# Kernel optimization log

Hardware: AMD Instinct MI355X
Metric: run time of the kernel (lower is better)

## Reference

```python
import jax, jax.numpy as jnp
import numpy as np

B, S, H, F, E, K = 4, 2048, 1024, 3584, 8, 2
CAP_FACTOR = 1.25


def setup_inputs() -> dict:
    key = jax.random.key(0)
    k1, k2, k3, k4, k5 = jax.random.split(key, 5)
    s_h = 1.0 / np.sqrt(H)
    s_f = 1.0 / np.sqrt(F)
    return {
        "hidden_states": jax.random.normal(k1, (B, S, H), dtype=jnp.float32),
        "gate_w": jax.random.normal(k2, (E, H), dtype=jnp.float32) * s_h,
        "w1": jax.random.normal(k3, (E, H, F), dtype=jnp.float32) * s_h,
        "w2": jax.random.normal(k4, (E, F, H), dtype=jnp.float32) * s_f,
        "w3": jax.random.normal(k5, (E, H, F), dtype=jnp.float32) * s_h,
    }


def _moe_forward(hidden_states, gate_w, w1, w2, w3):
    b, s, h = hidden_states.shape
    dtype = hidden_states.dtype
    x = hidden_states.reshape(-1, h)  # [B*S, H]
    router_logits = x @ gate_w.T  # [B*S, E]
    expert_weights = jax.nn.softmax(router_logits.astype(jnp.float32), axis=1)
    _, selected_experts = jax.lax.top_k(expert_weights, K)  # [B*S, K]

    top_k_idx = selected_experts.reshape(b, s, K)
    probs = expert_weights.reshape(b, s, E)

    capacity = int(s * K / E * CAP_FACTOR)  # expert capacity per batch

    # dispatch/combine masks (Mixtral 'dropping' implementation)
    expert_mask = jax.nn.one_hot(top_k_idx, E, dtype=jnp.int32)  # [b,s,K,E]
    mask_fused = expert_mask.reshape(b, s * K, E)
    count_fused = jnp.cumsum(mask_fused, axis=1)  # running count per expert
    count = count_fused.reshape(b, s, K, E)
    trunc_mask = expert_mask * (count <= capacity).astype(jnp.int32)
    combined_mask = trunc_mask.sum(axis=2)  # [b,s,E]
    masked_probs = probs * combined_mask  # drop over-capacity tokens

    pos_fused = mask_fused * count_fused
    pos = pos_fused.reshape(b, s, K, E)
    combined_pos = pos.sum(axis=2) * combined_mask  # [b,s,E], 1-based slot
    pos_in_cap = jax.nn.one_hot(combined_pos, capacity + 1, dtype=jnp.int32)
    combine_mask = masked_probs[..., None] * pos_in_cap  # [b,s,E,cap+1]
    combine_mask = combine_mask[..., 1:].astype(dtype)  # drop slot 0 (dropped tokens)
    dispatch_mask = (combine_mask != 0).astype(dtype)  # [b,s,E,cap]

    # dispatch tokens into per-expert capacity buffers
    dispatch = jnp.einsum('bsm,bsec->ebcm', hidden_states, dispatch_mask)
    # expert FFN (SwiGLU)
    h1 = jnp.einsum('ebcm,emh->ebch', dispatch, w1)
    h3 = jnp.einsum('ebcm,emh->ebch', dispatch, w3)
    expert_out = jnp.einsum('ebch,ehm->ebcm', jax.nn.silu(h1) * h3, w2)
    # combine back to token order with routing probabilities
    final = jnp.einsum('ebcm,bsec->bsm', expert_out, combine_mask)
    return final


def reference(hidden_states, gate_w, w1, w2, w3):
    return _moe_forward(hidden_states, gate_w, w1, w2, w3)
```

## Files before the change

### kernel.cpp

```cpp
#include <hip/hip_runtime.h>
#include <hip/hip_bf16.h>
#include <math.h>

#define B_   4
#define S_   2048
#define H_   1024
#define F_   3584
#define E_   8
#define TOPK 2
#define CAP  640
#define M_   (B_*CAP)
#define NTOK (B_*S_)

typedef __attribute__((ext_vector_type(8))) short short8;
typedef __attribute__((ext_vector_type(4))) float f32x4;
typedef __attribute__((ext_vector_type(4))) unsigned short us4;

static __device__ __forceinline__ unsigned short f2bf(float f) {
  __hip_bfloat16 h = __float2bfloat16(f);
  return *reinterpret_cast<unsigned short*>(&h);
}
static __device__ __forceinline__ float bf2f(unsigned short u) {
  unsigned int x = ((unsigned int)u) << 16;
  float f;
  __builtin_memcpy(&f, &x, 4);
  return f;
}

static __device__ __forceinline__ void gload16(const void* g, void* l) {
  __builtin_amdgcn_global_load_lds((const __attribute__((address_space(1))) void*)g,
                                   (__attribute__((address_space(3))) void*)l, 16, 0, 0);
}

#define BAR() __builtin_amdgcn_s_barrier()
#define WLG() asm volatile("s_waitcnt lgkmcnt(0)" ::: "memory")

__global__ __launch_bounds__(64) void k_router(const float* __restrict__ hs,
                                               const float* __restrict__ gw,
                                               int* __restrict__ e01,
                                               float* __restrict__ p01) {
  int t = blockIdx.x;
  int lane = threadIdx.x;
  const float4* xv = (const float4*)(hs + (size_t)t * H_);
  float4 xr[4];
#pragma unroll
  for (int i = 0; i < 4; ++i) xr[i] = xv[lane + i * 64];
  float logit[E_];
#pragma unroll
  for (int e = 0; e < E_; ++e) {
    const float4* gv = (const float4*)(gw + (size_t)e * H_);
    float acc = 0.f;
#pragma unroll
    for (int i = 0; i < 4; ++i) {
      float4 g = gv[lane + i * 64];
      acc += xr[i].x * g.x + xr[i].y * g.y + xr[i].z * g.z + xr[i].w * g.w;
    }
#pragma unroll
    for (int off = 32; off > 0; off >>= 1) acc += __shfl_xor(acc, off);
    logit[e] = acc;
  }
  float mx = logit[0];
#pragma unroll
  for (int e = 1; e < E_; ++e) mx = fmaxf(mx, logit[e]);
  float p[E_], s = 0.f;
#pragma unroll
  for (int e = 0; e < E_; ++e) { p[e] = expf(logit[e] - mx); s += p[e]; }
  float inv = 1.f / s;
  int e0 = 0;
#pragma unroll
  for (int e = 1; e < E_; ++e) if (p[e] > p[e0]) e0 = e;
  int e1 = (e0 == 0) ? 1 : 0;
#pragma unroll
  for (int e = 0; e < E_; ++e) if (e != e0 && p[e] > p[e1]) e1 = e;
  if (lane == 0) {
    e01[t * 2 + 0] = e0;
    e01[t * 2 + 1] = e1;
    p01[t * 2 + 0] = p[e0] * inv;
    p01[t * 2 + 1] = p[e1] * inv;
  }
}

__global__ __launch_bounds__(256) void k_positions(const int* __restrict__ e01,
                                                   int* __restrict__ pos,
                                                   int* __restrict__ disp) {
  int b = blockIdx.x, tid = threadIdx.x;
  __shared__ unsigned char eid[S_ * TOPK];
  __shared__ int part[256];
  for (int i = tid; i < E_ * CAP; i += 256)
    disp[((size_t)(i / CAP) * B_ + b) * CAP + (i % CAP)] = -1;
  for (int i = tid; i < S_ * TOPK; i += 256)
    eid[i] = (unsigned char)e01[b * S_ * TOPK + i];
  __syncthreads();
  const int per = (S_ * TOPK) / 256;
  int base = tid * per;
  for (int e = 0; e < E_; ++e) {
    int cnt = 0;
    for (int j = 0; j < per; ++j) cnt += (eid[base + j] == e) ? 1 : 0;
    part[tid] = cnt;
    __syncthreads();
    for (int off = 1; off < 256; off <<= 1) {
      int v = part[tid];
      int add = (tid >= off) ? part[tid - off] : 0;
      __syncthreads();
      part[tid] = v + add;
      __syncthreads();
    }
    int run = part[tid] - cnt;
    for (int j = 0; j < per; ++j) {
      int sl = base + j;
      if (eid[sl] == e) {
        ++run;
        int p = (run <= CAP) ? (run - 1) : -1;
        pos[b * S_ * TOPK + sl] = p;
        if (p >= 0) disp[((size_t)e * B_ + b) * CAP + p] = sl >> 1;
      }
    }
    __syncthreads();
  }
}

__global__ __launch_bounds__(256) void k_transpose(const float* __restrict__ in,
                                                   unsigned short* __restrict__ outp,
                                                   int R, int C, int ileave, int half,
                                                   size_t ostride_e) {
  __shared__ unsigned short ls[64][72];
  int e = blockIdx.z, tc = blockIdx.x, tr = blockIdx.y, tid = threadIdx.x;
  const float* src = in + (size_t)e * R * C + (size_t)tr * 64 * C + (size_t)tc * 64;
#pragma unroll
  for (int i = 0; i < 16; ++i) {
    int row = i * 4 + (tid >> 6), col = tid & 63;
    ls[row][col] = f2bf(src[(size_t)row * C + col]);
  }
  __syncthreads();
  unsigned short* dbase = outp + (size_t)e * ostride_e;
#pragma unroll
  for (int i = 0; i < 4; ++i) {
    int orow = i * 16 + (tid >> 4), oc = (tid & 15) * 4;
    int gr = tc * 64 + orow;
    int ri = ileave ? ((gr & ~15) * 2 + (gr & 15) + half * 16) : gr;
    us4 v = {ls[oc + 0][orow], ls[oc + 1][orow], ls[oc + 2][orow], ls[oc + 3][orow]};
    *(us4*)&dbase[(size_t)ri * R + tr * 64 + oc] = v;
  }
}

__global__ __launch_bounds__(256) void k_dispatch(const float* __restrict__ hs,
                                                  const int* __restrict__ disp,
                                                  unsigned short* __restrict__ xd) {
  int slot = blockIdx.x;
  int tid = threadIdx.x;
  int tok = disp[slot];
  int b = (slot / CAP) % B_;
  us4 v;
  if (tok >= 0) {
    const float4* src = (const float4*)(hs + ((size_t)b * S_ + tok) * H_);
    float4 f = src[tid];
    v = {f2bf(f.x), f2bf(f.y), f2bf(f.z), f2bf(f.w)};
  } else {
    v = {0, 0, 0, 0};
  }
  *(us4*)&xd[(size_t)slot * H_ + tid * 4] = v;
}

#define STAGE_A(d, h, t) {                                                    \
    int _ro = ((d) * 2 + (h)) * 8192 + tid * 8;                               \
    const unsigned short* _p = srcA + (size_t)(t) * 64 + (h) * 32;            \
    gload16(_p, &lds[_ro]);                                                   \
    gload16(_p + (size_t)128 * KTOT, &lds[_ro + 4096]);                       \
  }
#define STAGE_B(d, h, t) {                                                    \
    int _ro = 32768 + ((d) * 2 + (h)) * BREG + tid * 8;                       \
    const unsigned short* _p = srcB + (size_t)(t) * 64 + (h) * 32;            \
    gload16(_p, &lds[_ro]);                                                   \
    if (NREG == 4) gload16(_p + (size_t)128 * KTOT, &lds[_ro + 4096]);        \
  }
#define RD_A(d, h) {                                                          \
    const unsigned short* _pa = &lds[((d) * 2 + (h)) * 8192 + aoff];          \
    _Pragma("unroll") for (int m = 0; m < 8; ++m)                             \
      a[m] = *(const short8*)&_pa[m * 512];                                   \
  }
#define RD_B(d, h) {                                                          \
    const unsigned short* _pb = &lds[32768 + ((d) * 2 + (h)) * BREG + boff];  \
    _Pragma("unroll") for (int n = 0; n < NREG; ++n)                          \
      bfr[n] = *(const short8*)&_pb[n * 512];                                 \
  }
#define MFMA_ALL() {                                                          \
    __builtin_amdgcn_s_setprio(1);                                            \
    _Pragma("unroll") for (int m = 0; m < 8; ++m)                             \
      _Pragma("unroll") for (int n = 0; n < NREG; ++n)                        \
        acc[m][n] = __builtin_amdgcn_mfma_f32_16x16x32_bf16(a[m], bfr[n], acc[m][n], 0, 0, 0); \
    __builtin_amdgcn_s_setprio(0);                                            \
  }
#define WVM() {                                                               \
    if (NREG == 4) asm volatile("s_waitcnt vmcnt(8)" ::: "memory");           \
    else           asm volatile("s_waitcnt vmcnt(6)" ::: "memory");           \
  }
#define PHASE(pd, ph, sd, sh, st) {                                           \
    RD_A(pd, ph); RD_B(pd, ph);                                               \
    STAGE_A(sd, sh, st); STAGE_B(sd, sh, st);                                 \
    asm volatile("s_waitcnt lgkmcnt(8)" ::: "memory");                        \
    BAR(); WLG();                                                             \
    MFMA_ALL();                                                               \
    WVM(); BAR();                                                             \
  }

template <int KTOT, bool SWIGLU, int NREG, int MT, int NTN, int NTOTB>
__global__ __launch_bounds__(512, 2) void k_gemm256(const unsigned short* __restrict__ Aall,
                                                    const unsigned short* __restrict__ Ball,
                                                    unsigned short* __restrict__ Cout) {
  constexpr int NT = KTOT / 64;
  constexpr int NI = NT / 2;
  constexpr int BREG = 2048 * NREG;
  constexpr int LDS_US = 32768 + 4 * BREG;
  constexpr int BN = NREG * 64;
  __shared__ __align__(16) unsigned short lds[LDS_US];

  const int nwg = MT * NTN * E_;
  int lid = blockIdx.x;
  int sw = (lid & 7) * (nwg >> 3) + (lid >> 3);
  int e = sw / (MT * NTN);
  int rem = sw - e * (MT * NTN);
  int tn = rem / MT, tm = rem - tn * MT;

  int tid = threadIdx.x, li = tid & 63, wid = tid >> 6;
  int wm = wid >> 2, wn = wid & 3;

  int rS = tid >> 2;
  int gS = (tid & 3) ^ ((tid >> 3) & 3);
  const unsigned short* srcA = Aall + ((size_t)e * M_ + (size_t)tm * 256 + rS) * KTOT + gS * 8;
  const unsigned short* srcB = Ball + ((size_t)e * NTOTB + (size_t)tn * BN + rS) * KTOT + gS * 8;

  int sA = (li >> 4) ^ ((li >> 1) & 3);
  int aoff = (wm * 128 + (li & 15)) * 32 + sA * 8;
  int boff = (wn * (16 * NREG) + (li & 15)) * 32 + sA * 8;

  f32x4 acc[8][NREG] = {};
  short8 a[8], bfr[NREG];

  STAGE_A(0, 0, 0); STAGE_B(0, 0, 0);
  STAGE_A(0, 1, 0); STAGE_B(0, 1, 0);
  STAGE_A(1, 0, 1); STAGE_B(1, 0, 1);
  WVM();
  BAR();

#pragma unroll 1
  for (int i = 0; i < NI; ++i) {
    int t1 = 2 * i + 1;
    int t2 = (2 * i + 2 < NT) ? 2 * i + 2 : NT - 1;
    int t3 = (2 * i + 3 < NT) ? 2 * i + 3 : NT - 1;
    PHASE(0, 0, 1, 1, t1);
    PHASE(0, 1, 0, 0, t2);
    PHASE(1, 0, 0, 1, t2);
    PHASE(1, 1, 1, 0, t3);
  }

  int r0 = tm * 256 + wm * 128 + ((li >> 4) << 2);
  if constexpr (SWIGLU) {
    unsigned short* out = Cout + (size_t)e * M_ * F_;
#pragma unroll
    for (int m = 0; m < 8; ++m)
#pragma unroll
      for (int u = 0; u < 2; ++u) {
        int col = (tn * 8 + wn * 2 + u) * 16 + (li & 15);
#pragma unroll
        for (int j = 0; j < 4; ++j) {
          float h1 = acc[m][2 * u][j], h3 = acc[m][2 * u + 1][j];
          float sg = 1.f / (1.f + __expf(-h1));
          out[(size_t)(r0 + m * 16 + j) * F_ + col] = f2bf(h1 * sg * h3);
        }
      }
  } else {
    unsigned short* out = Cout + (size_t)e * M_ * NTOTB;
#pragma unroll
    for (int m = 0; m < 8; ++m)
#pragma unroll
      for (int n = 0; n < NREG; ++n) {
        int col = tn * BN + wn * (16 * NREG) + n * 16 + (li & 15);
#pragma unroll
        for (int j = 0; j < 4; ++j)
          out[(size_t)(r0 + m * 16 + j) * NTOTB + col] = f2bf(acc[m][n][j]);
      }
  }
}

__global__ __launch_bounds__(256) void k_combine(const unsigned short* __restrict__ Oe,
                                                 const int* __restrict__ e01,
                                                 const float* __restrict__ p01,
                                                 const int* __restrict__ pos,
                                                 float* __restrict__ outp) {
  int t = blockIdx.x;
  int b = t / S_;
  int tid = threadIdx.x;
  float4 acc = {0.f, 0.f, 0.f, 0.f};
#pragma unroll
  for (int k = 0; k < TOPK; ++k) {
    int p = pos[t * 2 + k];
    if (p >= 0) {
      int e = e01[t * 2 + k];
      float w = p01[t * 2 + k];
      size_t row = (size_t)e * M_ + (size_t)b * CAP + p;
      us4 v = *(const us4*)&Oe[row * H_ + tid * 4];
      acc.x += w * bf2f(v[0]);
      acc.y += w * bf2f(v[1]);
      acc.z += w * bf2f(v[2]);
      acc.w += w * bf2f(v[3]);
    }
  }
  *(float4*)&outp[(size_t)t * H_ + tid * 4] = acc;
}

extern "C" void kernel_launch(void* const* d_in, const int* in_sizes, int n_in,
                              void* d_out, int out_size, void* d_ws, size_t ws_size,
                              hipStream_t stream) {
  const float* hs = (const float*)d_in[0];
  const float* gw = (const float*)d_in[1];
  const float* w1 = (const float*)d_in[2];
  const float* w2 = (const float*)d_in[3];
  const float* w3 = (const float*)d_in[4];

  char* ws = (char*)d_ws;
  size_t off = 0;
  auto take = [&](size_t bytes) -> char* {
    char* p = ws + off;
    off += (bytes + 255) & ~(size_t)255;
    return p;
  };
  int*            e01  = (int*)take((size_t)NTOK * 2 * 4);
  float*          p01  = (float*)take((size_t)NTOK * 2 * 4);
  int*            pos  = (int*)take((size_t)NTOK * 2 * 4);
  int*            disp = (int*)take((size_t)E_ * B_ * CAP * 4);
  unsigned short* w13t = (unsigned short*)take((size_t)E_ * 2 * F_ * H_ * 2);
  unsigned short* w2t  = (unsigned short*)take((size_t)E_ * H_ * F_ * 2);
  unsigned short* xd   = (unsigned short*)take((size_t)E_ * M_ * H_ * 2);
  unsigned short* act  = (unsigned short*)take((size_t)E_ * M_ * F_ * 2);
  unsigned short* oe   = (unsigned short*)take((size_t)E_ * M_ * H_ * 2);

  k_router<<<NTOK, 64, 0, stream>>>(hs, gw, e01, p01);
  k_positions<<<B_, 256, 0, stream>>>(e01, pos, disp);
  k_transpose<<<dim3(F_ / 64, H_ / 64, E_), 256, 0, stream>>>(w1, w13t, H_, F_, 1, 0, (size_t)2 * F_ * H_);
  k_transpose<<<dim3(F_ / 64, H_ / 64, E_), 256, 0, stream>>>(w3, w13t, H_, F_, 1, 1, (size_t)2 * F_ * H_);
  k_transpose<<<dim3(H_ / 64, F_ / 64, E_), 256, 0, stream>>>(w2, w2t, F_, H_, 0, 0, (size_t)H_ * F_);
  k_dispatch<<<E_ * B_ * CAP, 256, 0, stream>>>(hs, disp, xd);
  k_gemm256<H_, true, 4, M_ / 256, (2 * F_) / 256, 2 * F_>
      <<<(M_ / 256) * ((2 * F_) / 256) * E_, 512, 0, stream>>>(xd, w13t, act);
  k_gemm256<F_, false, 2, M_ / 256, H_ / 128, H_>
      <<<(M_ / 256) * (H_ / 128) * E_, 512, 0, stream>>>(act, w2t, oe);
  k_combine<<<NTOK, 256, 0, stream>>>(oe, e01, p01, pos, (float*)d_out);
}
```

Baseline: 672.7 us.

## Use 256x256 tiles with split-K for down-projection and restructure GEMM pipeline

```diff
diff --git a/kernel.cpp b/kernel.cpp
--- a/kernel.cpp
+++ b/kernel.cpp
@@ -34,6 +34,8 @@
 
 #define BAR() __builtin_amdgcn_s_barrier()
 #define WLG() asm volatile("s_waitcnt lgkmcnt(0)" ::: "memory")
+#define VM4() asm volatile("s_waitcnt vmcnt(4)" ::: "memory")
+#define VM0() asm volatile("s_waitcnt vmcnt(0)" ::: "memory")
 
 __global__ __launch_bounds__(64) void k_router(const float* __restrict__ hs,
                                                const float* __restrict__ gw,
@@ -168,57 +170,45 @@
     gload16(_p + (size_t)128 * KTOT, &lds[_ro + 4096]);                       \
   }
 #define STAGE_B(d, h, t) {                                                    \
-    int _ro = 32768 + ((d) * 2 + (h)) * BREG + tid * 8;                       \
+    int _ro = 32768 + ((d) * 2 + (h)) * 8192 + tid * 8;                       \
     const unsigned short* _p = srcB + (size_t)(t) * 64 + (h) * 32;            \
     gload16(_p, &lds[_ro]);                                                   \
-    if (NREG == 4) gload16(_p + (size_t)128 * KTOT, &lds[_ro + 4096]);        \
-  }
-#define RD_A(d, h) {                                                          \
-    const unsigned short* _pa = &lds[((d) * 2 + (h)) * 8192 + aoff];          \
-    _Pragma("unroll") for (int m = 0; m < 8; ++m)                             \
-      a[m] = *(const short8*)&_pa[m * 512];                                   \
-  }
-#define RD_B(d, h) {                                                          \
-    const unsigned short* _pb = &lds[32768 + ((d) * 2 + (h)) * BREG + boff];  \
-    _Pragma("unroll") for (int n = 0; n < NREG; ++n)                          \
-      bfr[n] = *(const short8*)&_pb[n * 512];                                 \
-  }
-#define MFMA_ALL() {                                                          \
+    gload16(_p + (size_t)128 * KTOT, &lds[_ro + 4096]);                       \
+  }
+#define RD_A4(d, h, mh) {                                                     \
+    const unsigned short* _pa = &lds[((d) * 2 + (h)) * 8192 + aoff + (mh) * 2048]; \
+    _Pragma("unroll") for (int j = 0; j < 4; ++j)                             \
+      a[j] = *(const short8*)&_pa[j * 512];                                   \
+  }
+#define RD_B4(d, h) {                                                         \
+    const unsigned short* _pb = &lds[32768 + ((d) * 2 + (h)) * 8192 + boff];  \
+    _Pragma("unroll") for (int n = 0; n < 4; ++n)                             \
+      b[n] = *(const short8*)&_pb[n * 512];                                   \
+  }
+#define MFMA16(mh) {                                                          \
     __builtin_amdgcn_s_setprio(1);                                            \
-    _Pragma("unroll") for (int m = 0; m < 8; ++m)                             \
-      _Pragma("unroll") for (int n = 0; n < NREG; ++n)                        \
-        acc[m][n] = __builtin_amdgcn_mfma_f32_16x16x32_bf16(a[m], bfr[n], acc[m][n], 0, 0, 0); \
+    _Pragma("unroll") for (int j = 0; j < 4; ++j)                             \
+      _Pragma("unroll") for (int n = 0; n < 4; ++n)                           \
+        acc[(mh) * 4 + j][n] = __builtin_amdgcn_mfma_f32_16x16x32_bf16(a[j], b[n], acc[(mh) * 4 + j][n], 0, 0, 0); \
     __builtin_amdgcn_s_setprio(0);                                            \
   }
-#define WVM() {                                                               \
-    if (NREG == 4) asm volatile("s_waitcnt vmcnt(8)" ::: "memory");           \
-    else           asm volatile("s_waitcnt vmcnt(6)" ::: "memory");           \
-  }
-#define PHASE(pd, ph, sd, sh, st) {                                           \
-    RD_A(pd, ph); RD_B(pd, ph);                                               \
-    STAGE_A(sd, sh, st); STAGE_B(sd, sh, st);                                 \
-    asm volatile("s_waitcnt lgkmcnt(8)" ::: "memory");                        \
-    BAR(); WLG();                                                             \
-    MFMA_ALL();                                                               \
-    WVM(); BAR();                                                             \
-  }
-
-template <int KTOT, bool SWIGLU, int NREG, int MT, int NTN, int NTOTB>
+
+template <int KTOT, bool SWIGLU, int MT, int NTN, int NTOTB, int SPLITK>
 __global__ __launch_bounds__(512, 2) void k_gemm256(const unsigned short* __restrict__ Aall,
                                                     const unsigned short* __restrict__ Ball,
                                                     unsigned short* __restrict__ Cout) {
-  constexpr int NT = KTOT / 64;
-  constexpr int NI = NT / 2;
-  constexpr int BREG = 2048 * NREG;
-  constexpr int LDS_US = 32768 + 4 * BREG;
-  constexpr int BN = NREG * 64;
-  __shared__ __align__(16) unsigned short lds[LDS_US];
-
-  const int nwg = MT * NTN * E_;
+  constexpr int KSUB = KTOT / SPLITK;
+  constexpr int NT = KSUB / 64;
+  __shared__ __align__(16) unsigned short lds[65536];
+
+  const int nwg = MT * NTN * E_ * SPLITK;
   int lid = blockIdx.x;
   int sw = (lid & 7) * (nwg >> 3) + (lid >> 3);
-  int e = sw / (MT * NTN);
-  int rem = sw - e * (MT * NTN);
+  constexpr int PER = MT * NTN;
+  int ks = sw / (PER * E_);
+  int rem2 = sw - ks * (PER * E_);
+  int e = rem2 / PER;
+  int rem = rem2 - e * PER;
   int tn = rem / MT, tm = rem - tn * MT;
 
   int tid = threadIdx.x, li = tid & 63, wid = tid >> 6;
@@ -226,31 +216,43 @@
 
   int rS = tid >> 2;
   int gS = (tid & 3) ^ ((tid >> 3) & 3);
-  const unsigned short* srcA = Aall + ((size_t)e * M_ + (size_t)tm * 256 + rS) * KTOT + gS * 8;
-  const unsigned short* srcB = Ball + ((size_t)e * NTOTB + (size_t)tn * BN + rS) * KTOT + gS * 8;
+  const unsigned short* srcA = Aall + ((size_t)e * M_ + (size_t)tm * 256 + rS) * KTOT + ks * KSUB + gS * 8;
+  const unsigned short* srcB = Ball + ((size_t)e * NTOTB + (size_t)tn * 256 + rS) * KTOT + ks * KSUB + gS * 8;
 
   int sA = (li >> 4) ^ ((li >> 1) & 3);
   int aoff = (wm * 128 + (li & 15)) * 32 + sA * 8;
-  int boff = (wn * (16 * NREG) + (li & 15)) * 32 + sA * 8;
-
-  f32x4 acc[8][NREG] = {};
-  short8 a[8], bfr[NREG];
+  int boff = (wn * 64 + (li & 15)) * 32 + sA * 8;
+
+  f32x4 acc[8][4] = {};
+  short8 a[4], b[4];
 
   STAGE_A(0, 0, 0); STAGE_B(0, 0, 0);
   STAGE_A(0, 1, 0); STAGE_B(0, 1, 0);
-  STAGE_A(1, 0, 1); STAGE_B(1, 0, 1);
-  WVM();
+  VM4();
   BAR();
 
 #pragma unroll 1
-  for (int i = 0; i < NI; ++i) {
-    int t1 = 2 * i + 1;
-    int t2 = (2 * i + 2 < NT) ? 2 * i + 2 : NT - 1;
-    int t3 = (2 * i + 3 < NT) ? 2 * i + 3 : NT - 1;
-    PHASE(0, 0, 1, 1, t1);
-    PHASE(0, 1, 0, 0, t2);
-    PHASE(1, 0, 0, 1, t2);
-    PHASE(1, 1, 1, 0, t3);
+  for (int t = 0; t < NT - 1; ++t) {
+    int p = t & 1, q = p ^ 1;
+    RD_A4(p, 0, 0); RD_B4(p, 0); STAGE_A(q, 0, t + 1);
+    BAR(); WLG(); MFMA16(0); BAR();
+    RD_A4(p, 0, 1); STAGE_B(q, 0, t + 1); VM4();
+    BAR(); WLG(); MFMA16(1); BAR();
+    RD_A4(p, 1, 0); RD_B4(p, 1); STAGE_A(q, 1, t + 1);
+    BAR(); WLG(); MFMA16(0); BAR();
+    RD_A4(p, 1, 1); STAGE_B(q, 1, t + 1); VM4();
+    BAR(); WLG(); MFMA16(1); BAR();
+  }
+  {
+    int p = (NT - 1) & 1;
+    RD_A4(p, 0, 0); RD_B4(p, 0);
+    BAR(); WLG(); MFMA16(0); BAR();
+    RD_A4(p, 0, 1); VM0();
+    BAR(); WLG(); MFMA16(1); BAR();
+    RD_A4(p, 1, 0); RD_B4(p, 1);
+    BAR(); WLG(); MFMA16(0); BAR();
+    RD_A4(p, 1, 1);
+    BAR(); WLG(); MFMA16(1);
   }
 
   int r0 = tm * 256 + wm * 128 + ((li >> 4) << 2);
@@ -269,12 +271,12 @@
         }
       }
   } else {
-    unsigned short* out = Cout + (size_t)e * M_ * NTOTB;
+    unsigned short* out = Cout + ((size_t)ks * E_ + e) * M_ * NTOTB;
 #pragma unroll
     for (int m = 0; m < 8; ++m)
 #pragma unroll
-      for (int n = 0; n < NREG; ++n) {
-        int col = tn * BN + wn * (16 * NREG) + n * 16 + (li & 15);
+      for (int n = 0; n < 4; ++n) {
+        int col = tn * 256 + wn * 64 + n * 16 + (li & 15);
 #pragma unroll
         for (int j = 0; j < 4; ++j)
           out[(size_t)(r0 + m * 16 + j) * NTOTB + col] = f2bf(acc[m][n][j]);
@@ -282,7 +284,8 @@
   }
 }
 
-__global__ __launch_bounds__(256) void k_combine(const unsigned short* __restrict__ Oe,
+__global__ __launch_bounds__(256) void k_combine(const unsigned short* __restrict__ Oe0,
+                                                 const unsigned short* __restrict__ Oe1,
                                                  const int* __restrict__ e01,
                                                  const float* __restrict__ p01,
                                                  const int* __restrict__ pos,
@@ -298,11 +301,12 @@
       int e = e01[t * 2 + k];
       float w = p01[t * 2 + k];
       size_t row = (size_t)e * M_ + (size_t)b * CAP + p;
-      us4 v = *(const us4*)&Oe[row * H_ + tid * 4];
-      acc.x += w * bf2f(v[0]);
-      acc.y += w * bf2f(v[1]);
-      acc.z += w * bf2f(v[2]);
-      acc.w += w * bf2f(v[3]);
+      us4 v0 = *(const us4*)&Oe0[row * H_ + tid * 4];
+      us4 v1 = *(const us4*)&Oe1[row * H_ + tid * 4];
+      acc.x += w * (bf2f(v0[0]) + bf2f(v1[0]));
+      acc.y += w * (bf2f(v0[1]) + bf2f(v1[1]));
+      acc.z += w * (bf2f(v0[2]) + bf2f(v1[2]));
+      acc.w += w * (bf2f(v0[3]) + bf2f(v1[3]));
     }
   }
   *(float4*)&outp[(size_t)t * H_ + tid * 4] = acc;
@@ -332,7 +336,7 @@
   unsigned short* w2t  = (unsigned short*)take((size_t)E_ * H_ * F_ * 2);
   unsigned short* xd   = (unsigned short*)take((size_t)E_ * M_ * H_ * 2);
   unsigned short* act  = (unsigned short*)take((size_t)E_ * M_ * F_ * 2);
-  unsigned short* oe   = (unsigned short*)take((size_t)E_ * M_ * H_ * 2);
+  unsigned short* oe   = (unsigned short*)take((size_t)2 * E_ * M_ * H_ * 2);
 
   k_router<<<NTOK, 64, 0, stream>>>(hs, gw, e01, p01);
   k_positions<<<B_, 256, 0, stream>>>(e01, pos, disp);
@@ -340,9 +344,9 @@
   k_transpose<<<dim3(F_ / 64, H_ / 64, E_), 256, 0, stream>>>(w3, w13t, H_, F_, 1, 1, (size_t)2 * F_ * H_);
   k_transpose<<<dim3(H_ / 64, F_ / 64, E_), 256, 0, stream>>>(w2, w2t, F_, H_, 0, 0, (size_t)H_ * F_);
   k_dispatch<<<E_ * B_ * CAP, 256, 0, stream>>>(hs, disp, xd);
-  k_gemm256<H_, true, 4, M_ / 256, (2 * F_) / 256, 2 * F_>
+  k_gemm256<H_, true, M_ / 256, (2 * F_) / 256, 2 * F_, 1>
       <<<(M_ / 256) * ((2 * F_) / 256) * E_, 512, 0, stream>>>(xd, w13t, act);
-  k_gemm256<F_, false, 2, M_ / 256, H_ / 128, H_>
-      <<<(M_ / 256) * (H_ / 128) * E_, 512, 0, stream>>>(act, w2t, oe);
-  k_combine<<<NTOK, 256, 0, stream>>>(oe, e01, p01, pos, (float*)d_out);
-}
+  k_gemm256<F_, false, M_ / 256, H_ / 256, H_, 2>
+      <<<(M_ / 256) * (H_ / 256) * E_ * 2, 512, 0, stream>>>(act, w2t, oe);
+  k_combine<<<NTOK, 256, 0, stream>>>(oe, oe + (size_t)E_ * M_ * H_, e01, p01, pos, (float*)d_out);
+}
```

New measurement: 612.5 us. 9.0% less time.
